# Performance work log

Measured on AMD Instinct MI355X. Metric: run time of the kernel, lower is better.

## Reference

```python
import jax, jax.numpy as jnp
import numpy as np

N_NODES = 100000
N_EDGES = 1600000
IN_FEATS, HID, NUM_CLS = 128, 128, 40


def setup_inputs() -> dict:
    key = jax.random.key(0)
    ks = jax.random.split(key, 5)
    x = jax.random.normal(ks[0], (N_NODES, IN_FEATS), dtype=jnp.float32)
    # xavier-like scale for weights
    W1 = jax.random.normal(ks[1], (IN_FEATS, HID), dtype=jnp.float32) * (1.0 / np.sqrt(IN_FEATS))
    b1 = jnp.zeros((HID,), dtype=jnp.float32)
    W2 = jax.random.normal(ks[2], (HID, NUM_CLS), dtype=jnp.float32) * (1.0 / np.sqrt(HID))
    b2 = jnp.zeros((NUM_CLS,), dtype=jnp.float32)
    src = jax.random.randint(ks[3], (N_EDGES,), 0, N_NODES, dtype=jnp.int32)
    dst = jax.random.randint(ks[4], (N_EDGES,), 0, N_NODES, dtype=jnp.int32)
    return {"x": x, "W1": W1, "b1": b1, "W2": W2, "b2": b2, "src": src, "dst": dst}


def _graph_conv(h, W, b, src, dst, src_norm, dst_norm, n_nodes):
    # DGL GraphConv, norm='both': D_out^{-1/2} A D_in^{-1/2} H W + b
    # (weight-first vs aggregate-first ordering in DGL is mathematically identical)
    hs = h * src_norm[:, None]                      # [N, d] source-side norm
    msg = hs[src]                                   # [E, d] gather
    agg = jax.ops.segment_sum(msg, dst, num_segments=n_nodes)  # [N, d] scatter-add
    agg = agg * dst_norm[:, None]                   # dest-side norm
    return agg @ W + b


def reference(x, W1, b1, W2, b2, src, dst):
    n = x.shape[0]
    ones = jnp.ones(src.shape[0], dtype=x.dtype)
    out_deg = jnp.clip(jax.ops.segment_sum(ones, src, num_segments=n), 1.0)
    in_deg = jnp.clip(jax.ops.segment_sum(ones, dst, num_segments=n), 1.0)
    src_norm = out_deg ** -0.5
    dst_norm = in_deg ** -0.5
    h = jax.nn.relu(_graph_conv(x, W1, b1, src, dst, src_norm, dst_norm, n))
    return _graph_conv(h, W2, b2, src, dst, src_norm, dst_norm, n)
```

## Files before the change

### kernel.cpp

```cpp
#include <hip/hip_runtime.h>

constexpr int NN   = 100000;
constexpr int NE   = 1600000;
constexpr int INF  = 128;
constexpr int NC   = 40;

constexpr int BKSH = 9;
constexpr int NBK  = (NN + 511) / 512;
constexpr int CAPB = 10240;
constexpr int EPB  = 4096;
constexpr int PBLK = (NE + EPB - 1) / EPB;
constexpr int CVB  = 6250;

typedef __attribute__((ext_vector_type(8))) short short8;
typedef __attribute__((ext_vector_type(4))) float f32x4;

__device__ __forceinline__ float bflo(unsigned int u) { return __uint_as_float(u << 16); }
__device__ __forceinline__ float bfhi(unsigned int u) { return __uint_as_float(u & 0xffff0000u); }
__device__ __forceinline__ unsigned short f2bf(float f) {
    unsigned int u = __float_as_uint(f);
    return (unsigned short)((u + 0x7fffu + ((u >> 16) & 1u)) >> 16);
}
__device__ __forceinline__ unsigned int pack2(float a, float b) {
    return (unsigned int)f2bf(a) | ((unsigned int)f2bf(b) << 16);
}

__global__ __launch_bounds__(256) void partconv_kernel(const int* __restrict__ src,
                                                       const int* __restrict__ dst,
                                                       int* __restrict__ curD_g,
                                                       int* __restrict__ curS_g,
                                                       int* __restrict__ epartsD,
                                                       unsigned short* __restrict__ epartsS,
                                                       const float* __restrict__ x,
                                                       unsigned short* __restrict__ xh,
                                                       const float* __restrict__ W1,
                                                       const float* __restrict__ W2,
                                                       unsigned short* __restrict__ w1t,
                                                       unsigned short* __restrict__ w2t) {
    const int tid = threadIdx.x;
    if (blockIdx.x >= PBLK) {
        int cb = blockIdx.x - PBLK;
        if (cb < CVB) {
            int j = cb * 256 + tid;
            float4 v0 = ((const float4*)x)[2 * j];
            float4 v1 = ((const float4*)x)[2 * j + 1];
            uint4 o;
            o.x = pack2(v0.x, v0.y);
            o.y = pack2(v0.z, v0.w);
            o.z = pack2(v1.x, v1.y);
            o.w = pack2(v1.z, v1.w);
            ((uint4*)xh)[j] = o;
        } else if (cb == CVB) {
            for (int i = tid; i < 128 * 128; i += 256) {
                int k = i >> 7, n = i & 127;
                w1t[n * 128 + k] = f2bf(W1[i]);
            }
        } else {
            for (int i = tid; i < 48 * 128; i += 256) {
                int n = i >> 7, k = i & 127;
                w2t[i] = f2bf((n < NC) ? W2[k * NC + n] : 0.f);
            }
        }
        return;
    }
    __shared__ int sc[256];
    __shared__ int cntD[NBK], gadjD[NBK], curD[NBK];
    __shared__ int cntS[NBK], gadjS[NBK], curS[NBK];
    __shared__ int stageD[EPB];
    __shared__ unsigned short stageS[EPB];
    __shared__ unsigned char bidD[EPB];
    __shared__ unsigned char bidS[EPB];
    const int e0 = blockIdx.x * EPB;
    const int total = min(EPB, NE - e0);

    for (int i = tid; i < NBK; i += 256) { cntD[i] = 0; cntS[i] = 0; }
    __syncthreads();
    for (int i = tid; i < total; i += 256) {
        atomicAdd(&cntD[dst[e0 + i] >> BKSH], 1);
        atomicAdd(&cntS[src[e0 + i] >> BKSH], 1);
    }
    __syncthreads();
    {
        int v = (tid < NBK) ? cntD[tid] : 0;
        sc[tid] = v;
        __syncthreads();
        for (int off = 1; off < 256; off <<= 1) {
            int t = (tid >= off) ? sc[tid - off] : 0;
            __syncthreads();
            sc[tid] += t;
            __syncthreads();
        }
        if (tid < NBK) {
            int excl = sc[tid] - v;
            curD[tid] = excl;
            int g = (v > 0) ? atomicAdd(&curD_g[tid], v) : 0;
            gadjD[tid] = tid * CAPB + g - excl;
        }
        __syncthreads();
        v = (tid < NBK) ? cntS[tid] : 0;
        sc[tid] = v;
        __syncthreads();
        for (int off = 1; off < 256; off <<= 1) {
            int t = (tid >= off) ? sc[tid - off] : 0;
            __syncthreads();
            sc[tid] += t;
            __syncthreads();
        }
        if (tid < NBK) {
            int excl = sc[tid] - v;
            curS[tid] = excl;
            int g = (v > 0) ? atomicAdd(&curS_g[tid], v) : 0;
            gadjS[tid] = tid * CAPB + g - excl;
        }
    }
    __syncthreads();
    for (int i = tid; i < total; i += 256) {
        int s = src[e0 + i];
        int d = dst[e0 + i];
        int bD = d >> BKSH;
        int offD = atomicAdd(&curD[bD], 1);
        stageD[offD] = s | ((d - (bD << BKSH)) << 17);
        bidD[offD] = (unsigned char)bD;
        int bS = s >> BKSH;
        int offS = atomicAdd(&curS[bS], 1);
        stageS[offS] = (unsigned short)(s - (bS << BKSH));
        bidS[offS] = (unsigned char)bS;
    }
    __syncthreads();
    for (int j = tid; j < total; j += 256) {
        int b = bidD[j];
        epartsD[gadjD[b] + j] = stageD[j];
    }
    for (int j = tid; j < total; j += 256) {
        int b = bidS[j];
        epartsS[gadjS[b] + j] = stageS[j];
    }
}

__global__ __launch_bounds__(512) void pass2_kernel(const int* __restrict__ epartsD,
                                                    const unsigned short* __restrict__ epartsS,
                                                    const int* __restrict__ curD_g,
                                                    const int* __restrict__ curS_g,
                                                    int* __restrict__ row_beg,
                                                    int* __restrict__ row_end,
                                                    int* __restrict__ esrc,
                                                    float* __restrict__ srcn,
                                                    float* __restrict__ dstn) {
    __shared__ int hist[512];
    __shared__ int cur[512];
    __shared__ int histS[512];
    __shared__ int lesrc[CAPB];
    const int tid = threadIdx.x;
    const int b = blockIdx.x;

    const int base  = b * CAPB;
    const int cnt   = curD_g[b];
    const int cntS  = curS_g[b];
    const int n0 = b << BKSH;
    const int nloc = min(512, NN - n0);

    hist[tid] = 0;
    histS[tid] = 0;
    __syncthreads();
    for (int j = tid; j < cnt; j += 512)
        atomicAdd(&hist[epartsD[base + j] >> 17], 1);
    for (int j = tid; j < cntS; j += 512)
        atomicAdd(&histS[(int)epartsS[base + j]], 1);
    __syncthreads();
    int myc = hist[tid];
    int mycS = histS[tid];
    for (int off = 1; off < 512; off <<= 1) {
        int t = (tid >= off) ? hist[tid - off] : 0;
        __syncthreads();
        hist[tid] += t;
        __syncthreads();
    }
    int excl = hist[tid] - myc;
    cur[tid] = excl;
    if (tid < nloc) {
        int g = n0 + tid;
        row_beg[g] = base + excl;
        row_end[g] = base + excl + myc;
        dstn[g] = rsqrtf(fmaxf((float)myc, 1.0f));
        srcn[g] = rsqrtf(fmaxf((float)mycS, 1.0f));
    }
    __syncthreads();
    for (int j = tid; j < cnt; j += 512) {
        int rec = epartsD[base + j];
        int pos = atomicAdd(&cur[rec >> 17], 1);
        lesrc[pos] = rec & 0x1FFFF;
    }
    __syncthreads();
    for (int j = tid; j < cnt; j += 512) esrc[base + j] = lesrc[j];
}

__global__ __launch_bounds__(256, 8) void fused_kernel(const int* __restrict__ row_beg,
                                                       const int* __restrict__ row_end,
                                                       const int* __restrict__ esrc,
                                                       const unsigned short* __restrict__ xh,
                                                       const float* __restrict__ srcn,
                                                       const unsigned short* __restrict__ w1t,
                                                       const unsigned short* __restrict__ w2t,
                                                       const float* __restrict__ b1,
                                                       const float* __restrict__ dstn,
                                                       unsigned short* __restrict__ hwb) {
    __shared__ unsigned short At[32 * 128];
    __shared__ float dn[32], sn[32], b1l[128];
    const int tid  = threadIdx.x;
    const int r0   = blockIdx.x * 32;
    const int wv   = tid >> 6;
    const int lane = tid & 63;

    if (tid < 32) {
        int r = r0 + tid;
        dn[tid] = (r < NN) ? dstn[r] : 0.f;
        sn[tid] = (r < NN) ? srcn[r] : 0.f;
    }
    if (tid >= 64 && tid < 192) b1l[tid - 64] = b1[tid - 64];
    __syncthreads();

    const int quad = lane >> 4;
    const int l16  = lane & 15;
    for (int i = 0; i < 8; ++i) {
        const int node = r0 + wv * 8 + i;
        float a0 = 0.f, a1 = 0.f, a2 = 0.f, a3 = 0.f;
        float a4 = 0.f, a5 = 0.f, a6 = 0.f, a7 = 0.f;
        if (node < NN) {
            int beg = __builtin_amdgcn_readfirstlane(row_beg[node]);
            int end = __builtin_amdgcn_readfirstlane(row_end[node]);
            for (int e = beg; e < end; e += 16) {
                const int rem = end - e;
                int s[4];
#pragma unroll
                for (int t = 0; t < 4; ++t) {
                    int slot = t * 4 + quad;
                    s[t] = esrc[(slot < rem) ? (e + slot) : beg];
                }
                float n[4];
                uint4 u[4];
#pragma unroll
                for (int t = 0; t < 4; ++t) {
                    int slot = t * 4 + quad;
                    n[t] = (slot < rem) ? srcn[s[t]] : 0.f;
                    u[t] = ((const uint4*)(xh + (size_t)s[t] * INF))[l16];
                }
#pragma unroll
                for (int t = 0; t < 4; ++t) {
                    a0 += bflo(u[t].x) * n[t]; a1 += bfhi(u[t].x) * n[t];
                    a2 += bflo(u[t].y) * n[t]; a3 += bfhi(u[t].y) * n[t];
                    a4 += bflo(u[t].z) * n[t]; a5 += bfhi(u[t].z) * n[t];
                    a6 += bflo(u[t].w) * n[t]; a7 += bfhi(u[t].w) * n[t];
                }
            }
        }
        a0 += __shfl_down(a0, 32); a1 += __shfl_down(a1, 32);
        a2 += __shfl_down(a2, 32); a3 += __shfl_down(a3, 32);
        a4 += __shfl_down(a4, 32); a5 += __shfl_down(a5, 32);
        a6 += __shfl_down(a6, 32); a7 += __shfl_down(a7, 32);
        a0 += __shfl_down(a0, 16); a1 += __shfl_down(a1, 16);
        a2 += __shfl_down(a2, 16); a3 += __shfl_down(a3, 16);
        a4 += __shfl_down(a4, 16); a5 += __shfl_down(a5, 16);
        a6 += __shfl_down(a6, 16); a7 += __shfl_down(a7, 16);
        if (lane < 16) {
            uint4 o;
            o.x = pack2(a0, a1);
            o.y = pack2(a2, a3);
            o.z = pack2(a4, a5);
            o.w = pack2(a6, a7);
            *(uint4*)&At[(wv * 8 + i) * 128 + l16 * 8] = o;
        }
    }
    __syncthreads();

    const int lrow  = lane & 15;
    const int lquad = lane >> 4;
    const int rt    = wv >> 1;
    const int ntB   = (wv & 1) * 4;

    short8 afrag[4];
#pragma unroll
    for (int ks = 0; ks < 4; ++ks)
        afrag[ks] = *(const short8*)&At[(rt * 16 + lrow) * 128 + ks * 32 + lquad * 8];
    __syncthreads();

    float hreg[4][4];
#pragma unroll
    for (int nt2 = 0; nt2 < 4; ++nt2) {
        f32x4 acc = {0.f, 0.f, 0.f, 0.f};
#pragma unroll
        for (int ks = 0; ks < 4; ++ks) {
            short8 bfr = *(const short8*)&w1t[((ntB + nt2) * 16 + lrow) * 128 + ks * 32 + lquad * 8];
            acc = __builtin_amdgcn_mfma_f32_16x16x32_bf16(afrag[ks], bfr, acc, 0, 0, 0);
        }
#pragma unroll
        for (int i = 0; i < 4; ++i) hreg[nt2][i] = acc[i];
    }
#pragma unroll
    for (int nt2 = 0; nt2 < 4; ++nt2) {
        int col = (ntB + nt2) * 16 + lrow;
        float bb = b1l[col];
#pragma unroll
        for (int i = 0; i < 4; ++i) {
            int row = rt * 16 + lquad * 4 + i;
            At[row * 128 + col] = f2bf(fmaxf(hreg[nt2][i] * dn[row] + bb, 0.f));
        }
    }
    __syncthreads();

    if ((wv & 1) == 0) {
        short8 hf[4];
#pragma unroll
        for (int ks = 0; ks < 4; ++ks)
            hf[ks] = *(const short8*)&At[(rt * 16 + lrow) * 128 + ks * 32 + lquad * 8];
#pragma unroll
        for (int nt = 0; nt < 3; ++nt) {
            f32x4 acc = {0.f, 0.f, 0.f, 0.f};
#pragma unroll
            for (int ks = 0; ks < 4; ++ks) {
                short8 bfr = *(const short8*)&w2t[(nt * 16 + lrow) * 128 + ks * 32 + lquad * 8];
                acc = __builtin_amdgcn_mfma_f32_16x16x32_bf16(hf[ks], bfr, acc, 0, 0, 0);
            }
            int col = nt * 16 + lrow;
            if (col < NC) {
#pragma unroll
                for (int i = 0; i < 4; ++i) {
                    int row = rt * 16 + lquad * 4 + i;
                    int grow = r0 + row;
                    if (grow < NN)
                        hwb[(size_t)grow * NC + col] = f2bf(acc[i] * sn[row]);
                }
            }
        }
    }
}

__global__ __launch_bounds__(256) void gather2_kernel(const int* __restrict__ row_beg,
                                                      const int* __restrict__ row_end,
                                                      const int* __restrict__ esrc,
                                                      const unsigned short* __restrict__ hwb,
                                                      const float* __restrict__ dst_norm,
                                                      const float* __restrict__ b2,
                                                      float* __restrict__ out) {
    int node = (blockIdx.x * blockDim.x + threadIdx.x) >> 6;
    int lane = threadIdx.x & 63;
    if (node >= NN) return;
    int beg = __builtin_amdgcn_readfirstlane(row_beg[node]);
    int end = __builtin_amdgcn_readfirstlane(row_end[node]);
    const int g = lane / 10;
    const int j = lane - g * 10;
    const bool active = (g < 6);
    float4 acc = make_float4(0.f, 0.f, 0.f, 0.f);
    for (int e = beg; e < end; e += 18) {
        const int rem = end - e;
        int s[3];
        float m[3];
#pragma unroll
        for (int q = 0; q < 3; ++q) {
            int slot = q * 6 + g;
            bool v = active && (slot < rem);
            int idx = v ? (e + slot) : beg;
            s[q] = esrc[idx];
            m[q] = v ? 1.f : 0.f;
        }
        uint2 u[3];
#pragma unroll
        for (int q = 0; q < 3; ++q)
            u[q] = ((const uint2*)(hwb + (size_t)s[q] * NC))[j];
#pragma unroll
        for (int q = 0; q < 3; ++q) {
            acc.x += bflo(u[q].x) * m[q];
            acc.y += bfhi(u[q].x) * m[q];
            acc.z += bflo(u[q].y) * m[q];
            acc.w += bfhi(u[q].y) * m[q];
        }
    }
    float4 tot = acc;
#pragma unroll
    for (int k = 1; k < 6; ++k) {
        tot.x += __shfl(acc.x, j + 10 * k);
        tot.y += __shfl(acc.y, j + 10 * k);
        tot.z += __shfl(acc.z, j + 10 * k);
        tot.w += __shfl(acc.w, j + 10 * k);
    }
    if (lane < 10) {
        float dnv = dst_norm[node];
        float4 bb = ((const float4*)b2)[j];
        float4 o;
        o.x = tot.x * dnv + bb.x;
        o.y = tot.y * dnv + bb.y;
        o.z = tot.z * dnv + bb.z;
        o.w = tot.w * dnv + bb.w;
        ((float4*)(out + (size_t)node * NC))[j] = o;
    }
}

extern "C" void kernel_launch(void* const* d_in, const int* in_sizes, int n_in,
                              void* d_out, int out_size, void* d_ws, size_t ws_size,
                              hipStream_t stream) {
    const float* x   = (const float*)d_in[0];
    const float* W1  = (const float*)d_in[1];
    const float* b1  = (const float*)d_in[2];
    const float* W2  = (const float*)d_in[3];
    const float* b2  = (const float*)d_in[4];
    const int*   src = (const int*)d_in[5];
    const int*   dst = (const int*)d_in[6];
    float* out = (float*)d_out;

    float* srcn = (float*)d_ws;
    int* curDg = (int*)(srcn + NN);
    int* curSg = curDg + 256;
    int* row_beg = curSg + 256;
    int* row_end = row_beg + NN;
    float* dstn  = (float*)(row_end + NN);
    int* esrc    = (int*)(dstn + NN);
    size_t ofs = (size_t)NN + 512 + 3 * (size_t)NN + (size_t)NBK * CAPB;
    ofs = (ofs + 3) & ~(size_t)3;
    unsigned short* xh   = (unsigned short*)((float*)d_ws + ofs);
    unsigned short* w1t  = xh + (size_t)NN * INF;
    unsigned short* w2t  = w1t + 128 * 128;
    unsigned short* hwb  = w2t + 48 * 128;

    int* epartsD = (int*)d_out;
    unsigned short* epartsS = (unsigned short*)(epartsD + (size_t)NBK * CAPB);

    hipMemsetAsync(curDg, 0, 512 * sizeof(int), stream);

    partconv_kernel<<<PBLK + CVB + 2, 256, 0, stream>>>(src, dst, curDg, curSg,
                                                        epartsD, epartsS,
                                                        x, xh, W1, W2, w1t, w2t);
    pass2_kernel<<<NBK, 512, 0, stream>>>(epartsD, epartsS, curDg, curSg,
                                          row_beg, row_end, esrc, srcn, dstn);
    fused_kernel<<<(NN + 31) / 32, 256, 0, stream>>>(row_beg, row_end, esrc, xh,
                                                     srcn, w1t, w2t, b1, dstn, hwb);
    gather2_kernel<<<(NN * 64 + 255) / 256, 256, 0, stream>>>(row_beg, row_end,
                                                              esrc, hwb,
                                                              dstn, b2, out);
}
```

Before: 278.3 us.

## Pad layer-2 feature rows to 64 and gather with 16-byte loads

The intermediate layer-2 features are now stored with a 64-element (128-byte) row stride instead of 40. The second gather kernel uses 8 lanes per source row with uint4 loads and handles 8 edges per pass, then reduces with a shuffle tree. The fused kernel's LDS tile row stride is also padded from 128 to 136 to avoid bank conflicts. In exchange, each edge reads more bytes (padding columns are loaded and discarded) and the workspace for hwb grows, which must fit the existing allocation.

```diff
diff --git a/kernel.cpp b/kernel.cpp
--- a/kernel.cpp
+++ b/kernel.cpp
@@ -4,6 +4,7 @@
 constexpr int NE   = 1600000;
 constexpr int INF  = 128;
 constexpr int NC   = 40;
+constexpr int HPAD = 64;
 
 constexpr int BKSH = 9;
 constexpr int NBK  = (NN + 511) / 512;
@@ -11,6 +12,7 @@
 constexpr int EPB  = 4096;
 constexpr int PBLK = (NE + EPB - 1) / EPB;
 constexpr int CVB  = 6250;
+constexpr int ATS  = 136;
 
 typedef __attribute__((ext_vector_type(8))) short short8;
 typedef __attribute__((ext_vector_type(4))) float f32x4;
@@ -204,7 +206,7 @@
                                                        const float* __restrict__ b1,
                                                        const float* __restrict__ dstn,
                                                        unsigned short* __restrict__ hwb) {
-    __shared__ unsigned short At[32 * 128];
+    __shared__ unsigned short At[32 * ATS];
     __shared__ float dn[32], sn[32], b1l[128];
     const int tid  = threadIdx.x;
     const int r0   = blockIdx.x * 32;
@@ -267,7 +269,7 @@
             o.y = pack2(a2, a3);
             o.z = pack2(a4, a5);
             o.w = pack2(a6, a7);
-            *(uint4*)&At[(wv * 8 + i) * 128 + l16 * 8] = o;
+            *(uint4*)&At[(wv * 8 + i) * ATS + l16 * 8] = o;
         }
     }
     __syncthreads();
@@ -280,7 +282,7 @@
     short8 afrag[4];
 #pragma unroll
     for (int ks = 0; ks < 4; ++ks)
-        afrag[ks] = *(const short8*)&At[(rt * 16 + lrow) * 128 + ks * 32 + lquad * 8];
+        afrag[ks] = *(const short8*)&At[(rt * 16 + lrow) * ATS + ks * 32 + lquad * 8];
     __syncthreads();
 
     float hreg[4][4];
@@ -302,7 +304,7 @@
 #pragma unroll
         for (int i = 0; i < 4; ++i) {
             int row = rt * 16 + lquad * 4 + i;
-            At[row * 128 + col] = f2bf(fmaxf(hreg[nt2][i] * dn[row] + bb, 0.f));
+            At[row * ATS + col] = f2bf(fmaxf(hreg[nt2][i] * dn[row] + bb, 0.f));
         }
     }
     __syncthreads();
@@ -311,7 +313,7 @@
         short8 hf[4];
 #pragma unroll
         for (int ks = 0; ks < 4; ++ks)
-            hf[ks] = *(const short8*)&At[(rt * 16 + lrow) * 128 + ks * 32 + lquad * 8];
+            hf[ks] = *(const short8*)&At[(rt * 16 + lrow) * ATS + ks * 32 + lquad * 8];
 #pragma unroll
         for (int nt = 0; nt < 3; ++nt) {
             f32x4 acc = {0.f, 0.f, 0.f, 0.f};
@@ -327,7 +329,7 @@
                     int row = rt * 16 + lquad * 4 + i;
                     int grow = r0 + row;
                     if (grow < NN)
-                        hwb[(size_t)grow * NC + col] = f2bf(acc[i] * sn[row]);
+                        hwb[(size_t)grow * HPAD + col] = f2bf(acc[i] * sn[row]);
                 }
             }
         }
@@ -346,51 +348,61 @@
     if (node >= NN) return;
     int beg = __builtin_amdgcn_readfirstlane(row_beg[node]);
     int end = __builtin_amdgcn_readfirstlane(row_end[node]);
-    const int g = lane / 10;
-    const int j = lane - g * 10;
-    const bool active = (g < 6);
-    float4 acc = make_float4(0.f, 0.f, 0.f, 0.f);
-    for (int e = beg; e < end; e += 18) {
+    const int g = lane >> 3;
+    const int j = lane & 7;
+    float a0 = 0.f, a1 = 0.f, a2 = 0.f, a3 = 0.f;
+    float a4 = 0.f, a5 = 0.f, a6 = 0.f, a7 = 0.f;
+    for (int e = beg; e < end; e += 24) {
         const int rem = end - e;
         int s[3];
         float m[3];
 #pragma unroll
         for (int q = 0; q < 3; ++q) {
-            int slot = q * 6 + g;
-            bool v = active && (slot < rem);
-            int idx = v ? (e + slot) : beg;
-            s[q] = esrc[idx];
+            int slot = q * 8 + g;
+            bool v = (slot < rem);
+            s[q] = esrc[v ? (e + slot) : beg];
             m[q] = v ? 1.f : 0.f;
         }
-        uint2 u[3];
+        uint4 u[3];
 #pragma unroll
         for (int q = 0; q < 3; ++q)
-            u[q] = ((const uint2*)(hwb + (size_t)s[q] * NC))[j];
+            u[q] = ((const uint4*)(hwb + (size_t)s[q] * HPAD))[j];
 #pragma unroll
         for (int q = 0; q < 3; ++q) {
-            acc.x += bflo(u[q].x) * m[q];
-            acc.y += bfhi(u[q].x) * m[q];
-            acc.z += bflo(u[q].y) * m[q];
-            acc.w += bfhi(u[q].y) * m[q];
-        }
-    }
-    float4 tot = acc;
-#pragma unroll
-    for (int k = 1; k < 6; ++k) {
-        tot.x += __shfl(acc.x, j + 10 * k);
-        tot.y += __shfl(acc.y, j + 10 * k);
-        tot.z += __shfl(acc.z, j + 10 * k);
-        tot.w += __shfl(acc.w, j + 10 * k);
-    }
-    if (lane < 10) {
+            a0 += bflo(u[q].x) * m[q]; a1 += bfhi(u[q].x) * m[q];
+            a2 += bflo(u[q].y) * m[q]; a3 += bfhi(u[q].y) * m[q];
+            a4 += bflo(u[q].z) * m[q]; a5 += bfhi(u[q].z) * m[q];
+            a6 += bflo(u[q].w) * m[q]; a7 += bfhi(u[q].w) * m[q];
+        }
+    }
+    a0 += __shfl_down(a0, 32); a1 += __shfl_down(a1, 32);
+    a2 += __shfl_down(a2, 32); a3 += __shfl_down(a3, 32);
+    a4 += __shfl_down(a4, 32); a5 += __shfl_down(a5, 32);
+    a6 += __shfl_down(a6, 32); a7 += __shfl_down(a7, 32);
+    a0 += __shfl_down(a0, 16); a1 += __shfl_down(a1, 16);
+    a2 += __shfl_down(a2, 16); a3 += __shfl_down(a3, 16);
+    a4 += __shfl_down(a4, 16); a5 += __shfl_down(a5, 16);
+    a6 += __shfl_down(a6, 16); a7 += __shfl_down(a7, 16);
+    a0 += __shfl_down(a0, 8);  a1 += __shfl_down(a1, 8);
+    a2 += __shfl_down(a2, 8);  a3 += __shfl_down(a3, 8);
+    a4 += __shfl_down(a4, 8);  a5 += __shfl_down(a5, 8);
+    a6 += __shfl_down(a6, 8);  a7 += __shfl_down(a7, 8);
+    if (lane < 5) {
         float dnv = dst_norm[node];
-        float4 bb = ((const float4*)b2)[j];
-        float4 o;
-        o.x = tot.x * dnv + bb.x;
-        o.y = tot.y * dnv + bb.y;
-        o.z = tot.z * dnv + bb.z;
-        o.w = tot.w * dnv + bb.w;
-        ((float4*)(out + (size_t)node * NC))[j] = o;
+        float4 bb0 = ((const float4*)b2)[2 * lane];
+        float4 bb1 = ((const float4*)b2)[2 * lane + 1];
+        float4 o0, o1;
+        o0.x = a0 * dnv + bb0.x;
+        o0.y = a1 * dnv + bb0.y;
+        o0.z = a2 * dnv + bb0.z;
+        o0.w = a3 * dnv + bb0.w;
+        o1.x = a4 * dnv + bb1.x;
+        o1.y = a5 * dnv + bb1.y;
+        o1.z = a6 * dnv + bb1.z;
+        o1.w = a7 * dnv + bb1.w;
+        float4* op = (float4*)(out + (size_t)node * NC);
+        op[2 * lane]     = o0;
+        op[2 * lane + 1] = o1;
     }
 }
 
```

New measurement: 275.3 us. No clear change (-1.1%).
